# Kernel optimization log

Hardware: AMD Instinct MI355X
Metric: run time of the kernel (lower is better)

## Reference

```python
import jax, jax.numpy as jnp
import numpy as np

N = 50000      # nodes
E = 800000     # edges per sampled adjacency
F_IN = 128     # input features
H = 256        # hidden
C = 112        # classes (ogbn-proteins)
L = 8          # num_layers
EPS = 1e-5     # BatchNorm eps


def setup_inputs() -> dict:
    key = jax.random.key(0)
    ks = jax.random.split(key, 8)
    x = jax.random.normal(ks[0], (N, F_IN), dtype=jnp.float32)
    edge1 = jax.random.randint(ks[1], (2, E), 0, N)
    edge2 = jax.random.randint(ks[2], (2, E), 0, N)
    in_W = jax.random.normal(ks[3], (F_IN, H), dtype=jnp.float32) * 0.05
    in_b = jnp.zeros((H,), jnp.float32)
    convW = jax.random.normal(ks[4], (L, H, H), dtype=jnp.float32) * 0.05
    convB = jnp.zeros((L, H), jnp.float32)
    bn_gamma = jnp.ones((L, H), jnp.float32)
    bn_beta = jnp.zeros((L, H), jnp.float32)
    out_W = jax.random.normal(ks[5], (H, C), dtype=jnp.float32) * 0.05
    out_b = jnp.zeros((C,), jnp.float32)
    layer_w = jax.random.normal(ks[6], (L,), dtype=jnp.float32)
    return dict(x=x, edge1=edge1, edge2=edge2, in_W=in_W, in_b=in_b,
                convW=convW, convB=convB, bn_gamma=bn_gamma, bn_beta=bn_beta,
                out_W=out_W, out_b=out_b, layer_w=layer_w)


def _gcn_norm(edge_index):
    # GCNConv default: add self-loops, sym-normalize D^{-1/2} A_hat D^{-1/2}.
    loops = jnp.arange(N)
    row = jnp.concatenate([edge_index[0], loops])  # source
    col = jnp.concatenate([edge_index[1], loops])  # target
    deg = jax.ops.segment_sum(jnp.ones_like(row, jnp.float32), col, num_segments=N)
    dinv = jnp.where(deg > 0, jax.lax.rsqrt(deg), 0.0)
    return row, col, dinv[row] * dinv[col]


def reference(x, edge1, edge2, in_W, in_b, convW, convB, bn_gamma, bn_beta,
              out_W, out_b, layer_w):
    adj1 = _gcn_norm(edge1)
    adj2 = _gcn_norm(edge2)
    h = x @ in_W + in_b                                  # input_fc: [N, H]
    w = jax.nn.softmax(layer_w)                          # residual layer weights
    acc = jnp.zeros_like(h)
    for i in range(L):
        row, col, norm = adj1 if i < L // 2 else adj2
        t = h @ convW[i] + convB[i]                      # GCNConv linear
        msg = t[row] * norm[:, None]                     # gather + scale  [E+N, H]
        h = jax.ops.segment_sum(msg, col, num_segments=N)  # scatter-add SpMM
        mu = h.mean(axis=0)                              # BatchNorm1d (batch stats)
        var = h.var(axis=0)
        h = (h - mu) * jax.lax.rsqrt(var + EPS) * bn_gamma[i] + bn_beta[i]
        h = jax.nn.relu(h)                               # dropout is identity in eval
        acc = acc + w[i] * h                             # weighted residual sum
    out = acc @ out_W + out_b                            # out_fc: [N, C]
    return jax.nn.log_softmax(out, axis=1)
```

## Files before the change

kernel.cpp:

```cpp
#include <hip/hip_runtime.h>
#include <math.h>

#define NN 50000
#define HH 256
#define FIN 128
#define CC 112
#define LL 8
#define EE 800000
#define EPSB 1e-5f
#define NGRP 8
#define NPG (NN / NGRP)
#define SLW 32
#define NSL (HH / SLW)

typedef unsigned short u16;
typedef unsigned int u32;
typedef __attribute__((ext_vector_type(8))) short bf16x8;
typedef __attribute__((ext_vector_type(4))) float f32x4;

__device__ __forceinline__ u16 f2bf(float f) {
    u32 u = __float_as_uint(f);
    u32 r = (u + 0x7FFFu + ((u >> 16) & 1u)) >> 16;
    return (u16)r;
}
__device__ __forceinline__ float bflo(u32 u) { return __uint_as_float(u << 16); }
__device__ __forceinline__ float bfhi(u32 u) { return __uint_as_float(u & 0xFFFF0000u); }
__device__ __forceinline__ float bf1(u16 u) { return __uint_as_float(((u32)u) << 16); }

__device__ __forceinline__ void gload16(const u16* g, u16* l) {
    __builtin_amdgcn_global_load_lds(
        (const __attribute__((address_space(1))) void*)g,
        (__attribute__((address_space(3))) void*)l, 16, 0, 0);
}

__global__ __launch_bounds__(256) void k_fill2(const int* __restrict__ ed1,
                                               const int* __restrict__ ed2,
                                               int* __restrict__ cur,
                                               u16* __restrict__ src1p,
                                               u16* __restrict__ src2p) {
    const int g = blockIdx.x & 7;
    const int bg = blockIdx.x >> 3;
    const int nthr = (gridDim.x >> 3) * 256;
    const int tid = bg * 256 + threadIdx.x;
    const int lo = g * NPG;

    for (int e = tid; e < EE; e += nthr) {
        int c = __builtin_nontemporal_load(ed1 + e + EE);
        if ((u32)(c - lo) < (u32)NPG) {
            int r = __builtin_nontemporal_load(ed1 + e);
            int pos = atomicAdd(&cur[c], 1);
            src1p[(c << 6) + pos] = (u16)r;
        }
    }
    for (int e = tid; e < EE; e += nthr) {
        int c = __builtin_nontemporal_load(ed2 + e + EE);
        if ((u32)(c - lo) < (u32)NPG) {
            int r = __builtin_nontemporal_load(ed2 + e);
            int pos = atomicAdd(&cur[NN + c], 1);
            src2p[(c << 6) + pos] = (u16)r;
        }
    }
}

__global__ void k_dinv2(const int* __restrict__ deg, float* __restrict__ dinv1,
                        float* __restrict__ dinv2, int n) {
    int v = blockIdx.x * blockDim.x + threadIdx.x;
    if (v >= 2 * n) return;
    float* d = (v < n) ? dinv1 : dinv2;
    int vv = (v < n) ? v : v - n;
    d[vv] = rsqrtf((float)(deg[v] + 1));
}

__global__ void k_wt(const float* __restrict__ W, u16* __restrict__ Wt, int K, int N) {
    __shared__ u16 sm[32][33];
    const float* Wl = W + (size_t)blockIdx.z * K * N;
    u16* Wtl = Wt + (size_t)blockIdx.z * K * N;
    int k0 = blockIdx.y * 32, n0 = blockIdx.x * 32;
    int tx = threadIdx.x, ty = threadIdx.y;
#pragma unroll
    for (int r = 0; r < 32; r += 8)
        sm[ty + r][tx] = f2bf(Wl[(size_t)(k0 + ty + r) * N + n0 + tx]);
    __syncthreads();
#pragma unroll
    for (int r = 0; r < 32; r += 8)
        Wtl[(size_t)(n0 + ty + r) * K + k0 + tx] = sm[tx][ty + r];
}

__global__ void k_outwt(const float* __restrict__ outW, const float* __restrict__ outb,
                        u16* __restrict__ outWt, float* __restrict__ obb) {
    int idx = blockIdx.x * 256 + threadIdx.x;
    if (idx >= 128 * 256) return;
    int n = idx >> 8, k = idx & 255;
    float v = (n < CC) ? outW[(size_t)k * CC + n] : 0.f;
    outWt[(size_t)n * HH + k] = f2bf(v);
    if (idx < 128) obb[idx] = (idx < CC) ? outb[idx] : 0.f;
}

__global__ void k_xcast(const float* __restrict__ x, u16* __restrict__ xb, int n4) {
    int i = blockIdx.x * blockDim.x + threadIdx.x;
    if (i >= n4) return;
    float4 v = ((const float4*)x)[i];
    ushort4 o;
    o.x = f2bf(v.x); o.y = f2bf(v.y); o.z = f2bf(v.z); o.w = f2bf(v.w);
    *(ushort4*)(xb + ((size_t)i << 2)) = o;
}

template <bool F32OUT, bool SWIZ, bool SLICED>
__global__ __launch_bounds__(256) void k_gemm_bf16(const u16* __restrict__ A,
                                                   const u16* __restrict__ Bt,
                                                   const float* __restrict__ bias,
                                                   const float* __restrict__ rowscale,
                                                   void* __restrict__ Cout,
                                                   int M, int Nc, int K) {
    int m0, n0;
    if (SWIZ) {
        int id = blockIdx.x;
        int g = id >> 4, r = id & 15;
        int m = g * 8 + (r & 7);
        if (m * 128 >= M) return;
        m0 = m * 128;
        n0 = (r >> 3) * 128;
    } else {
        m0 = blockIdx.x * 128;
        n0 = 0;
    }
    __shared__ u16 As[128 * 32];
    __shared__ u16 Bs[128 * 32];
    const int tid = threadIdx.x;
    const int w = tid >> 6, lane = tid & 63;
    const int wr = (w >> 1) * 64, wc = (w & 1) * 64;
    const int lm = lane & 15, lq = lane >> 4;

    f32x4 acc[4][4];
#pragma unroll
    for (int i = 0; i < 4; ++i)
#pragma unroll
        for (int j = 0; j < 4; ++j) acc[i][j] = (f32x4){0.f, 0.f, 0.f, 0.f};

    const int srow = w * 16 + (lane >> 2);
    const int scol = (lane & 3) * 8;

    for (int k0 = 0; k0 < K; k0 += 32) {
        int gm = m0 + srow;        if (gm >= M) gm = M - 1;
        gload16(A + (size_t)gm * K + k0 + scol, As + (size_t)(w * 64) * 8);
        int gm2 = m0 + 64 + srow;  if (gm2 >= M) gm2 = M - 1;
        gload16(A + (size_t)gm2 * K + k0 + scol, As + (size_t)(256 + w * 64) * 8);
        gload16(Bt + (size_t)(n0 + srow) * K + k0 + scol, Bs + (size_t)(w * 64) * 8);
        gload16(Bt + (size_t)(n0 + 64 + srow) * K + k0 + scol, Bs + (size_t)(256 + w * 64) * 8);
        __syncthreads();

        bf16x8 af[4], bfr[4];
#pragma unroll
        for (int i = 0; i < 4; ++i)
            af[i] = *(const bf16x8*)(As + (wr + i * 16 + lm) * 32 + lq * 8);
#pragma unroll
        for (int j = 0; j < 4; ++j)
            bfr[j] = *(const bf16x8*)(Bs + (wc + j * 16 + lm) * 32 + lq * 8);
#pragma unroll
        for (int i = 0; i < 4; ++i)
#pragma unroll
            for (int j = 0; j < 4; ++j)
                acc[i][j] = __builtin_amdgcn_mfma_f32_16x16x32_bf16(af[i], bfr[j], acc[i][j], 0, 0, 0);
        __syncthreads();
    }

#pragma unroll
    for (int j = 0; j < 4; ++j) {
        int gc = n0 + wc + j * 16 + lm;
        float bj = (gc < Nc) ? bias[gc] : 0.f;
#pragma unroll
        for (int i = 0; i < 4; ++i) {
#pragma unroll
            for (int r = 0; r < 4; ++r) {
                int gr = m0 + wr + i * 16 + lq * 4 + r;
                if (gr < M && gc < Nc) {
                    float rs = rowscale ? rowscale[gr] : 1.0f;
                    float val = (acc[i][j][r] + bj) * rs;
                    if (F32OUT)
                        ((float*)Cout)[(size_t)gr * Nc + gc] = val;
                    else if (SLICED)
                        ((u16*)Cout)[((size_t)(gc >> 5) * M + gr) * SLW + (gc & 31)] = f2bf(val);
                    else
                        ((u16*)Cout)[(size_t)gr * Nc + gc] = f2bf(val);
                }
            }
        }
    }
}

__global__ __launch_bounds__(512) void k_spmm_sl8(const u16* __restrict__ ts,
                                                  const int* __restrict__ deg,
                                                  const u16* __restrict__ srcp,
                                                  const float* __restrict__ dinv,
                                                  u16* __restrict__ hpre,
                                                  float* __restrict__ bns,
                                                  float* __restrict__ bnq) {
    __shared__ float lsum[8][SLW];
    __shared__ float lsq[8][SLW];
    const int s = blockIdx.x & 7;
    const int nb = blockIdx.x >> 3;
    const int w = threadIdx.x >> 6;
    const int lane = threadIdx.x & 63;
    const int sub = lane >> 3;
    const int li = lane & 7;
    const u16* tsl = ts + (size_t)s * NN * SLW + li * 4;

    const int v = nb * 64 + w * 8 + sub;
    float4 ssum = make_float4(0.f, 0.f, 0.f, 0.f);
    float4 ssq  = make_float4(0.f, 0.f, 0.f, 0.f);

    if (v < NN) {
        const u16* src = srcp + ((size_t)v << 6);
        const float dv = dinv[v];
        uint2 a = *(const uint2*)(tsl + (size_t)v * SLW);
        float4 A;
        A.x = bflo(a.x); A.y = bfhi(a.x); A.z = bflo(a.y); A.w = bfhi(a.y);
        int end = deg[v];
        int j = 0;
        for (; j + 16 <= end; j += 16) {
            uint4 sp0 = *(const uint4*)(src + j);
            uint4 sp1 = *(const uint4*)(src + j + 8);
            uint2 b0 = *(const uint2*)(tsl + (size_t)(sp0.x & 0xFFFFu) * SLW);
            uint2 b1 = *(const uint2*)(tsl + (size_t)(sp0.x >> 16) * SLW);
            uint2 b2 = *(const uint2*)(tsl + (size_t)(sp0.y & 0xFFFFu) * SLW);
            uint2 b3 = *(const uint2*)(tsl + (size_t)(sp0.y >> 16) * SLW);
            uint2 b4 = *(const uint2*)(tsl + (size_t)(sp0.z & 0xFFFFu) * SLW);
            uint2 b5 = *(const uint2*)(tsl + (size_t)(sp0.z >> 16) * SLW);
            uint2 b6 = *(const uint2*)(tsl + (size_t)(sp0.w & 0xFFFFu) * SLW);
            uint2 b7 = *(const uint2*)(tsl + (size_t)(sp0.w >> 16) * SLW);
            uint2 c0 = *(const uint2*)(tsl + (size_t)(sp1.x & 0xFFFFu) * SLW);
            uint2 c1 = *(const uint2*)(tsl + (size_t)(sp1.x >> 16) * SLW);
            uint2 c2 = *(const uint2*)(tsl + (size_t)(sp1.y & 0xFFFFu) * SLW);
            uint2 c3 = *(const uint2*)(tsl + (size_t)(sp1.y >> 16) * SLW);
            uint2 c4 = *(const uint2*)(tsl + (size_t)(sp1.z & 0xFFFFu) * SLW);
            uint2 c5 = *(const uint2*)(tsl + (size_t)(sp1.z >> 16) * SLW);
            uint2 c6 = *(const uint2*)(tsl + (size_t)(sp1.w & 0xFFFFu) * SLW);
            uint2 c7 = *(const uint2*)(tsl + (size_t)(sp1.w >> 16) * SLW);
            A.x += bflo(b0.x) + bflo(b1.x) + bflo(b2.x) + bflo(b3.x)
                 + bflo(b4.x) + bflo(b5.x) + bflo(b6.x) + bflo(b7.x)
                 + bflo(c0.x) + bflo(c1.x) + bflo(c2.x) + bflo(c3.x)
                 + bflo(c4.x) + bflo(c5.x) + bflo(c6.x) + bflo(c7.x);
            A.y += bfhi(b0.x) + bfhi(b1.x) + bfhi(b2.x) + bfhi(b3.x)
                 + bfhi(b4.x) + bfhi(b5.x) + bfhi(b6.x) + bfhi(b7.x)
                 + bfhi(c0.x) + bfhi(c1.x) + bfhi(c2.x) + bfhi(c3.x)
                 + bfhi(c4.x) + bfhi(c5.x) + bfhi(c6.x) + bfhi(c7.x);
            A.z += bflo(b0.y) + bflo(b1.y) + bflo(b2.y) + bflo(b3.y)
                 + bflo(b4.y) + bflo(b5.y) + bflo(b6.y) + bflo(b7.y)
                 + bflo(c0.y) + bflo(c1.y) + bflo(c2.y) + bflo(c3.y)
                 + bflo(c4.y) + bflo(c5.y) + bflo(c6.y) + bflo(c7.y);
            A.w += bfhi(b0.y) + bfhi(b1.y) + bfhi(b2.y) + bfhi(b3.y)
                 + bfhi(b4.y) + bfhi(b5.y) + bfhi(b6.y) + bfhi(b7.y)
                 + bfhi(c0.y) + bfhi(c1.y) + bfhi(c2.y) + bfhi(c3.y)
                 + bfhi(c4.y) + bfhi(c5.y) + bfhi(c6.y) + bfhi(c7.y);
        }
        for (; j + 8 <= end; j += 8) {
            uint4 sp = *(const uint4*)(src + j);
            uint2 b0 = *(const uint2*)(tsl + (size_t)(sp.x & 0xFFFFu) * SLW);
            uint2 b1 = *(const uint2*)(tsl + (size_t)(sp.x >> 16) * SLW);
            uint2 b2 = *(const uint2*)(tsl + (size_t)(sp.y & 0xFFFFu) * SLW);
            uint2 b3 = *(const uint2*)(tsl + (size_t)(sp.y >> 16) * SLW);
            uint2 b4 = *(const uint2*)(tsl + (size_t)(sp.z & 0xFFFFu) * SLW);
            uint2 b5 = *(const uint2*)(tsl + (size_t)(sp.z >> 16) * SLW);
            uint2 b6 = *(const uint2*)(tsl + (size_t)(sp.w & 0xFFFFu) * SLW);
            uint2 b7 = *(const uint2*)(tsl + (size_t)(sp.w >> 16) * SLW);
            A.x += bflo(b0.x) + bflo(b1.x) + bflo(b2.x) + bflo(b3.x)
                 + bflo(b4.x) + bflo(b5.x) + bflo(b6.x) + bflo(b7.x);
            A.y += bfhi(b0.x) + bfhi(b1.x) + bfhi(b2.x) + bfhi(b3.x)
                 + bfhi(b4.x) + bfhi(b5.x) + bfhi(b6.x) + bfhi(b7.x);
            A.z += bflo(b0.y) + bflo(b1.y) + bflo(b2.y) + bflo(b3.y)
                 + bflo(b4.y) + bflo(b5.y) + bflo(b6.y) + bflo(b7.y);
            A.w += bfhi(b0.y) + bfhi(b1.y) + bfhi(b2.y) + bfhi(b3.y)
                 + bfhi(b4.y) + bfhi(b5.y) + bfhi(b6.y) + bfhi(b7.y);
        }
        for (; j + 2 <= end; j += 2) {
            int s0 = src[j], s1 = src[j + 1];
            uint2 b0 = *(const uint2*)(tsl + (size_t)s0 * SLW);
            uint2 b1 = *(const uint2*)(tsl + (size_t)s1 * SLW);
            A.x += bflo(b0.x) + bflo(b1.x);
            A.y += bfhi(b0.x) + bfhi(b1.x);
            A.z += bflo(b0.y) + bflo(b1.y);
            A.w += bfhi(b0.y) + bfhi(b1.y);
        }
        if (j < end) {
            uint2 b0 = *(const uint2*)(tsl + (size_t)src[j] * SLW);
            A.x += bflo(b0.x); A.y += bfhi(b0.x);
            A.z += bflo(b0.y); A.w += bfhi(b0.y);
        }
        ushort4 o;
        o.x = f2bf(A.x * dv); o.y = f2bf(A.y * dv);
        o.z = f2bf(A.z * dv); o.w = f2bf(A.w * dv);
        *(ushort4*)(hpre + (size_t)v * HH + s * SLW + li * 4) = o;
        float fx = bf1(o.x), fy = bf1(o.y), fz = bf1(o.z), fw = bf1(o.w);
        ssum.x = fx; ssum.y = fy; ssum.z = fz; ssum.w = fw;
        ssq.x = fx * fx; ssq.y = fy * fy; ssq.z = fz * fz; ssq.w = fw * fw;
    }

#pragma unroll
    for (int d = 8; d < 64; d <<= 1) {
        ssum.x += __shfl_xor(ssum.x, d, 64);
        ssum.y += __shfl_xor(ssum.y, d, 64);
        ssum.z += __shfl_xor(ssum.z, d, 64);
        ssum.w += __shfl_xor(ssum.w, d, 64);
        ssq.x += __shfl_xor(ssq.x, d, 64);
        ssq.y += __shfl_xor(ssq.y, d, 64);
        ssq.z += __shfl_xor(ssq.z, d, 64);
        ssq.w += __shfl_xor(ssq.w, d, 64);
    }
    if (lane < 8) {
        *(float4*)&lsum[w][lane * 4] = ssum;
        *(float4*)&lsq[w][lane * 4] = ssq;
    }
    __syncthreads();
    int t = threadIdx.x;
    if (t < SLW) {
        float a = 0.f;
#pragma unroll
        for (int ww = 0; ww < 8; ++ww) a += lsum[ww][t];
        atomicAdd(&bns[(nb & 7) * HH + s * SLW + t], a);
    } else if (t < 2 * SLW) {
        int c = t - SLW;
        float a = 0.f;
#pragma unroll
        for (int ww = 0; ww < 8; ++ww) a += lsq[ww][c];
        atomicAdd(&bnq[(nb & 7) * HH + s * SLW + c], a);
    }
}

__global__ __launch_bounds__(256) void k_bnnorm(const u16* __restrict__ hpre,
                         u16* __restrict__ accb, u16* __restrict__ hb,
                         const float* __restrict__ bins,
                         const float* __restrict__ gamma, const float* __restrict__ beta,
                         const float* __restrict__ wArr, int layer) {
    __shared__ float sscale[HH], sshift[HH];
    const float invN = 1.0f / (float)NN;
    {
        int tcol = threadIdx.x;
        float m = 0.f, qq = 0.f;
#pragma unroll
        for (int b = 0; b < 8; ++b) {
            m += bins[b * HH + tcol];
            qq += bins[(8 + b) * HH + tcol];
        }
        m *= invN;
        float var = qq * invN - m * m;
        float sc = rsqrtf(var + EPSB) * gamma[tcol];
        sscale[tcol] = sc;
        sshift[tcol] = beta[tcol] - m * sc;
    }
    __syncthreads();
    int idx = blockIdx.x * blockDim.x + threadIdx.x;
    if (idx >= NN * (HH / 4)) return;
    int c = (idx & 63) << 2;
    float w = wArr[layer];
    ushort4 hv = ((const ushort4*)hpre)[idx];
    ushort4 av = ((const ushort4*)accb)[idx];
    u16* hp = &hv.x;
    u16* ap = &av.x;
    ushort4 oh, oa;
    u16* ohp = &oh.x;
    u16* oap = &oa.x;
#pragma unroll
    for (int k = 0; k < 4; ++k) {
        float v = fmaf(bf1(hp[k]), sscale[c + k], sshift[c + k]);
        v = fmaxf(v, 0.f);
        oap[k] = f2bf(fmaf(w, v, bf1(ap[k])));
        ohp[k] = f2bf(v);
    }
    ((ushort4*)accb)[idx] = oa;
    *(ushort4*)(hb + ((size_t)idx << 2)) = oh;
}

__global__ void k_softmaxw(const float* __restrict__ lw, float* __restrict__ wArr) {
    if (threadIdx.x == 0 && blockIdx.x == 0) {
        float m = -3.0e38f;
        for (int i = 0; i < LL; ++i) m = fmaxf(m, lw[i]);
        float e[LL]; float sum = 0.f;
        for (int i = 0; i < LL; ++i) { e[i] = expf(lw[i] - m); sum += e[i]; }
        for (int i = 0; i < LL; ++i) wArr[i] = e[i] / sum;
    }
}

__global__ __launch_bounds__(256) void k_logsoftmax(const float* __restrict__ z,
                                                    float* __restrict__ out) {
    int gt = blockIdx.x * blockDim.x + threadIdx.x;
    int v = gt >> 6;
    int lane = threadIdx.x & 63;
    if (v >= NN) return;
    const float* row = z + (size_t)v * CC;
    float v0 = row[lane];
    float v1 = (lane + 64 < CC) ? row[lane + 64] : -3.0e38f;
    float m = fmaxf(v0, v1);
#pragma unroll
    for (int d = 1; d < 64; d <<= 1) m = fmaxf(m, __shfl_xor(m, d, 64));
    float e = expf(v0 - m) + ((lane + 64 < CC) ? expf(v1 - m) : 0.f);
#pragma unroll
    for (int d = 1; d < 64; d <<= 1) e += __shfl_xor(e, d, 64);
    float lse = m + logf(e);
    out[(size_t)v * CC + lane] = v0 - lse;
    if (lane + 64 < CC) out[(size_t)v * CC + lane + 64] = v1 - lse;
}

extern "C" void kernel_launch(void* const* d_in, const int* in_sizes, int n_in,
                              void* d_out, int out_size, void* d_ws, size_t ws_size,
                              hipStream_t stream) {
    const float* x     = (const float*)d_in[0];
    const int*   e1    = (const int*)d_in[1];
    const int*   e2    = (const int*)d_in[2];
    const float* inW   = (const float*)d_in[3];
    const float* inb   = (const float*)d_in[4];
    const float* convW = (const float*)d_in[5];
    const float* convB = (const float*)d_in[6];
    const float* gamma = (const float*)d_in[7];
    const float* beta  = (const float*)d_in[8];
    const float* outW  = (const float*)d_in[9];
    const float* outb  = (const float*)d_in[10];
    const float* lw    = (const float*)d_in[11];

    char* ws = (char*)d_ws;
    size_t off = 0;
    auto alloc = [&](size_t bytes) -> void* {
        void* p = ws + off;
        off = (off + bytes + 255) & ~(size_t)255;
        return p;
    };
    u16*   hb    = (u16*)alloc((size_t)NN * HH * 2);
    u16*   tb    = (u16*)alloc((size_t)NN * HH * 2);
    u16*   hpre  = (u16*)alloc((size_t)NN * HH * 2);
    u16*   accb  = (u16*)alloc((size_t)NN * HH * 2);
    u16*   convWt= (u16*)alloc((size_t)LL * HH * HH * 2);
    u16*   inWt  = (u16*)alloc((size_t)HH * FIN * 2);
    u16*   outWt = (u16*)alloc((size_t)128 * HH * 2);
    float* obb   = (float*)alloc(128 * 4);
    float* dinv1 = (float*)alloc((size_t)NN * 4);
    float* dinv2 = (float*)alloc((size_t)NN * 4);
    u16*   src1p = (u16*)alloc((size_t)NN * 64 * 2);
    u16*   src2p = (u16*)alloc((size_t)NN * 64 * 2);
    int*   curz  = (int*)alloc((size_t)2 * NN * 4);
    float* bnsq  = (float*)alloc((size_t)LL * 16 * HH * 4);
    float* wArr  = (float*)alloc(64);
    u16*   xb    = tb;
    float* logits = (float*)hpre;

    int* cur1 = curz;

    hipMemsetAsync(curz, 0, (size_t)2 * NN * 4, stream);
    hipMemsetAsync(bnsq, 0, (size_t)LL * 16 * HH * 4, stream);
    hipMemsetAsync(accb, 0, (size_t)NN * HH * 2, stream);

    k_fill2<<<8 * 256, 256, 0, stream>>>(e1, e2, curz, src1p, src2p);
    k_dinv2<<<(2 * NN + 255) / 256, 256, 0, stream>>>(curz, dinv1, dinv2, NN);

    k_softmaxw<<<1, 64, 0, stream>>>(lw, wArr);

    {
        dim3 g(HH / 32, HH / 32, LL);
        dim3 b(32, 8);
        k_wt<<<g, b, 0, stream>>>(convW, convWt, HH, HH);
        dim3 g2(HH / 32, FIN / 32, 1);
        k_wt<<<g2, b, 0, stream>>>(inW, inWt, FIN, HH);
        k_outwt<<<128, 256, 0, stream>>>(outW, outb, outWt, obb);
    }
    k_xcast<<<(NN * FIN / 4 + 255) / 256, 256, 0, stream>>>(x, xb, NN * FIN / 4);

    const int MT = (NN + 127) / 128;
    const int GSW = ((MT + 7) / 8) * 16;
    k_gemm_bf16<false, true, false><<<GSW, 256, 0, stream>>>(xb, inWt, inb, nullptr, hb,
                                                             NN, HH, FIN);

    const int NBL = (NN + 63) / 64;
    const int SPB = NBL * NSL;
    const int ELB = (NN * (HH / 4) + 255) / 256;
    for (int i = 0; i < LL; ++i) {
        const int* dg = (i < LL / 2) ? cur1 : (curz + NN);
        const u16* sr = (i < LL / 2) ? src1p : src2p;
        const float* dv = (i < LL / 2) ? dinv1 : dinv2;
        float* bins = bnsq + (size_t)i * 16 * HH;
        k_gemm_bf16<false, true, true><<<GSW, 256, 0, stream>>>(hb,
                                                          convWt + (size_t)i * HH * HH,
                                                          convB + (size_t)i * HH, dv, tb,
                                                          NN, HH, HH);
        k_spmm_sl8<<<SPB, 512, 0, stream>>>(tb, dg, sr, dv, hpre, bins, bins + 8 * HH);
        k_bnnorm<<<ELB, 256, 0, stream>>>(hpre, accb, hb, bins,
                                          gamma + (size_t)i * HH, beta + (size_t)i * HH,
                                          wArr, i);
    }

    k_gemm_bf16<true, false, false><<<MT, 256, 0, stream>>>(accb, outWt, obb, nullptr, logits,
                                                            NN, CC, HH);
    k_logsoftmax<<<NN / 4, 256, 0, stream>>>(logits, (float*)d_out);
}
```

Measured before the change: 1.175 ms.

## Partition edges into per-group buckets before CSR fill

Replaces the fill kernel, where each of the 8 node groups rescanned the full edge arrays, with a two-pass scheme. A partition kernel bins packed (col,row) pairs into 16 buckets using a shared-memory histogram and global offsets. A second kernel then scatters each bucket into the padded adjacency lists. This removes the 8x redundant reads of the edge arrays, at the cost of an extra intermediate buffer, a fixed bucket capacity, and one more launch.

```diff
diff --git a/kernel.cpp b/kernel.cpp
--- a/kernel.cpp
+++ b/kernel.cpp
@@ -12,6 +12,7 @@
 #define NPG (NN / NGRP)
 #define SLW 32
 #define NSL (HH / SLW)
+#define BCAP 110000
 
 typedef unsigned short u16;
 typedef unsigned int u32;
@@ -33,32 +34,60 @@
         (__attribute__((address_space(3))) void*)l, 16, 0, 0);
 }
 
-__global__ __launch_bounds__(256) void k_fill2(const int* __restrict__ ed1,
-                                               const int* __restrict__ ed2,
+__global__ __launch_bounds__(256) void k_part(const int* __restrict__ ed1,
+                                              const int* __restrict__ ed2,
+                                              int* __restrict__ bcnt,
+                                              u32* __restrict__ bucket) {
+    __shared__ int hist[16], base[16], cnt2[16];
+    const int t = threadIdx.x;
+    if (t < 16) { hist[t] = 0; cnt2[t] = 0; }
+    __syncthreads();
+    const int e0 = blockIdx.x * 2048;
+    int myb[8]; u32 myp[8];
+#pragma unroll
+    for (int k = 0; k < 8; ++k) {
+        int e = e0 + k * 256 + t;
+        myb[k] = -1;
+        if (e < 2 * EE) {
+            const int* ed = (e < EE) ? ed1 : ed2;
+            int ee = (e < EE) ? e : e - EE;
+            int c = ed[ee + EE];
+            int r = ed[ee];
+            int b = ((e >= EE) ? 8 : 0) | (c / NPG);
+            myb[k] = b;
+            myp[k] = ((u32)c << 16) | (u32)r;
+            atomicAdd(&hist[b], 1);
+        }
+    }
+    __syncthreads();
+    if (t < 16) base[t] = atomicAdd(&bcnt[t], hist[t]);
+    __syncthreads();
+#pragma unroll
+    for (int k = 0; k < 8; ++k) {
+        if (myb[k] >= 0) {
+            int off = atomicAdd(&cnt2[myb[k]], 1);
+            bucket[(size_t)myb[k] * BCAP + base[myb[k]] + off] = myp[k];
+        }
+    }
+}
+
+__global__ __launch_bounds__(256) void k_fillB(const u32* __restrict__ bucket,
+                                               const int* __restrict__ bcnt,
                                                int* __restrict__ cur,
                                                u16* __restrict__ src1p,
                                                u16* __restrict__ src2p) {
-    const int g = blockIdx.x & 7;
-    const int bg = blockIdx.x >> 3;
-    const int nthr = (gridDim.x >> 3) * 256;
-    const int tid = bg * 256 + threadIdx.x;
-    const int lo = g * NPG;
-
-    for (int e = tid; e < EE; e += nthr) {
-        int c = __builtin_nontemporal_load(ed1 + e + EE);
-        if ((u32)(c - lo) < (u32)NPG) {
-            int r = __builtin_nontemporal_load(ed1 + e);
-            int pos = atomicAdd(&cur[c], 1);
-            src1p[(c << 6) + pos] = (u16)r;
-        }
-    }
-    for (int e = tid; e < EE; e += nthr) {
-        int c = __builtin_nontemporal_load(ed2 + e + EE);
-        if ((u32)(c - lo) < (u32)NPG) {
-            int r = __builtin_nontemporal_load(ed2 + e);
-            int pos = atomicAdd(&cur[NN + c], 1);
-            src2p[(c << 6) + pos] = (u16)r;
-        }
+    const int b = blockIdx.x & 15;
+    const int n = bcnt[b];
+    u16* sp = (b < 8) ? src1p : src2p;
+    int* cu = (b < 8) ? cur : cur + NN;
+    const u32* bk = bucket + (size_t)b * BCAP;
+    const int stride = (gridDim.x >> 4) * 256;
+    for (int i = (blockIdx.x >> 4) * 256 + threadIdx.x; i < n; i += stride) {
+        u32 p = bk[i];
+        int c = p >> 16;
+        int r = p & 0xFFFFu;
+        int pos = atomicAdd(&cu[c], 1);
+        sp[(c << 6) + pos] = (u16)r;
     }
 }
 
@@ -438,6 +467,8 @@
     int*   curz  = (int*)alloc((size_t)2 * NN * 4);
     float* bnsq  = (float*)alloc((size_t)LL * 16 * HH * 4);
     float* wArr  = (float*)alloc(64);
+    u32*   bucket= (u32*)alloc((size_t)16 * BCAP * 4);
+    int*   bcnt  = (int*)alloc(16 * 4);
     u16*   xb    = tb;
     float* logits = (float*)hpre;
 
@@ -446,8 +477,10 @@
     hipMemsetAsync(curz, 0, (size_t)2 * NN * 4, stream);
     hipMemsetAsync(bnsq, 0, (size_t)LL * 16 * HH * 4, stream);
     hipMemsetAsync(accb, 0, (size_t)NN * HH * 2, stream);
-
-    k_fill2<<<8 * 256, 256, 0, stream>>>(e1, e2, curz, src1p, src2p);
+    hipMemsetAsync(bcnt, 0, 16 * 4, stream);
+
+    k_part<<<(2 * EE + 2047) / 2048, 256, 0, stream>>>(e1, e2, bcnt, bucket);
+    k_fillB<<<16 * 64, 256, 0, stream>>>(bucket, bcnt, curz, src1p, src2p);
     k_dinv2<<<(2 * NN + 255) / 256, 256, 0, stream>>>(curz, dinv1, dinv2, NN);
 
     k_softmaxw<<<1, 64, 0, stream>>>(lw, wArr);
```

Result: no change. 1.185 ms (+0.8%).
